# Optimization experiments

Hardware: AMD Instinct MI355X
Metric: run time of the kernel (lower is better)

Reference implementation:

```python
import jax, jax.numpy as jnp
import numpy as np

D_MODEL = 1024
NHEAD = 16
D_K = D_MODEL // NHEAD


def setup_inputs() -> dict:
    key = jax.random.key(0)
    ks = jax.random.split(key, 9)
    s = 1.0 / np.sqrt(D_MODEL)
    return {
        "x": jax.random.normal(ks[0], (4, 2048, D_MODEL), dtype=jnp.float32),
        "Wq": jax.random.uniform(ks[1], (D_MODEL, D_MODEL), jnp.float32, -s, s),
        "bq": jax.random.uniform(ks[2], (D_MODEL,), jnp.float32, -s, s),
        "Wk": jax.random.uniform(ks[3], (D_MODEL, D_MODEL), jnp.float32, -s, s),
        "bk": jax.random.uniform(ks[4], (D_MODEL,), jnp.float32, -s, s),
        "Wv": jax.random.uniform(ks[5], (D_MODEL, D_MODEL), jnp.float32, -s, s),
        "bv": jax.random.uniform(ks[6], (D_MODEL,), jnp.float32, -s, s),
        "Wo": jax.random.uniform(ks[7], (D_MODEL, D_MODEL), jnp.float32, -s, s),
        "bo": jax.random.uniform(ks[8], (D_MODEL,), jnp.float32, -s, s),
    }


def reference(x, Wq, bq, Wk, bk, Wv, bv, Wo, bo):
    B, S, D = x.shape
    H, dk = NHEAD, D_K

    def split_heads(t):  # [B,S,D] -> [B,H,S,dk]
        return t.reshape(B, S, H, dk).transpose(0, 2, 1, 3)

    q = split_heads(x @ Wq + bq)
    k = split_heads(x @ Wk + bk)
    v = split_heads(x @ Wv + bv)

    scores = jnp.einsum('bhqd,bhkd->bhqk', q, k) / jnp.sqrt(jnp.float32(dk))
    attn = jax.nn.softmax(scores, axis=-1)
    out = jnp.einsum('bhqk,bhkd->bhqd', attn, v)  # [B,H,S,dk]
    out = out.transpose(0, 2, 1, 3).reshape(B, S, D)
    return out @ Wo + bo
```

## Files before the change

### kernel.cpp

```cpp
#include <hip/hip_runtime.h>


typedef short short8 __attribute__((ext_vector_type(8)));
typedef float f32x4 __attribute__((ext_vector_type(4)));
typedef float f32x16 __attribute__((ext_vector_type(16)));

#define DMODEL 1024
#define NH 16
#define DK 64
#define SEQ 2048
#define NB 4
#define MTOT (NB*SEQ)
#define KSCALE 0.18033688f

__device__ __forceinline__ unsigned short f2bf(float f) {
    union { float f; unsigned u; } v; v.f = f;
    unsigned r = (v.u + 0x7FFFu + ((v.u >> 16) & 1u)) >> 16;
    return (unsigned short)r;
}

__device__ __forceinline__ unsigned pk2(float a, float b) {
    unsigned r;
    asm("v_cvt_pk_bf16_f32 %0, %1, %2" : "=v"(r) : "v"(a), "v"(b));
    return r;
}

__device__ __forceinline__ float exp2a(float x) {
    float r; asm("v_exp_f32 %0, %1" : "=v"(r) : "v"(x)); return r;
}

__device__ __forceinline__ float max3a(float a, float b, float c) {
    float r; asm("v_max3_f32 %0, %1, %2, %3" : "=v"(r) : "v"(a), "v"(b), "v"(c)); return r;
}

__device__ __forceinline__ void plswap(unsigned &a, unsigned &b) {
    asm volatile("v_permlane32_swap_b32 %0, %1" : "+v"(a), "+v"(b));
}

__device__ __forceinline__ void gload16(const short* g, short* l) {
    __builtin_amdgcn_global_load_lds(
        (const __attribute__((address_space(1))) unsigned*)(const void*)g,
        (__attribute__((address_space(3))) unsigned*)(void*)l,
        16, 0, 0);
}

union Frag { short8 s8; unsigned u[4]; };

__global__ __launch_bounds__(256) void cvt_kernel(const float* __restrict__ in,
                                                  short* __restrict__ out, int n4) {
    int i = blockIdx.x * 256 + threadIdx.x;
    if (i >= n4) return;
    float4 v = ((const float4*)in)[i];
    short4 o;
    o.x = (short)f2bf(v.x); o.y = (short)f2bf(v.y);
    o.z = (short)f2bf(v.z); o.w = (short)f2bf(v.w);
    ((short4*)out)[i] = o;
}

__global__ __launch_bounds__(256) void transpose_kernel(const float* __restrict__ W,
                                                        short* __restrict__ Wt) {
    __shared__ float t[32][33];
    int r0 = blockIdx.y * 32, c0 = blockIdx.x * 32;
    int tr = threadIdx.x >> 3;
    int tc = (threadIdx.x & 7) * 4;
    float4 v = *(const float4*)&W[(r0 + tr) * DMODEL + c0 + tc];
    t[tr][tc + 0] = v.x; t[tr][tc + 1] = v.y; t[tr][tc + 2] = v.z; t[tr][tc + 3] = v.w;
    __syncthreads();
    short4 o;
    o.x = (short)f2bf(t[tc + 0][tr]);
    o.y = (short)f2bf(t[tc + 1][tr]);
    o.z = (short)f2bf(t[tc + 2][tr]);
    o.w = (short)f2bf(t[tc + 3][tr]);
    *(short4*)&Wt[(c0 + tr) * DMODEL + r0 + tc] = o;
}

template<int MODE>
__global__ __launch_bounds__(256) void gemm_kernel(
    const short* __restrict__ A, const short* __restrict__ Bt,
    const float* __restrict__ b0, const float* __restrict__ b1, const float* __restrict__ b2,
    short* __restrict__ Qb, short* __restrict__ Kb, short* __restrict__ Vtb,
    float* __restrict__ Cout)
{
    __shared__ __align__(16) short As[128 * 64];
    __shared__ __align__(16) short Bs[128 * 64];
    const int K = DMODEL;
    int m0 = blockIdx.y * 128, n0 = blockIdx.x * 128;
    int tid = threadIdx.x, lane = tid & 63, wid = tid >> 6;
    int wm = (wid >> 1) * 64, wn = (wid & 1) * 64;

    int srow = 8 * wid + (lane >> 3);
    int scol = ((lane & 7) ^ (lane >> 3)) * 8;
    const short* aSrc = A + (size_t)(m0 + srow) * K + scol;
    const short* bSrc = Bt + (size_t)(n0 + srow) * K + scol;

    f32x4 acc[4][4];
    #pragma unroll
    for (int i = 0; i < 4; i++)
        #pragma unroll
        for (int j = 0; j < 4; j++) acc[i][j] = (f32x4){0.f, 0.f, 0.f, 0.f};

    for (int kt = 0; kt < K; kt += 64) {
        #pragma unroll
        for (int i = 0; i < 4; ++i) {
            gload16(aSrc + (size_t)(32 * i) * K + kt, &As[(8 * wid + 32 * i) * 64]);
            gload16(bSrc + (size_t)(32 * i) * K + kt, &Bs[(8 * wid + 32 * i) * 64]);
        }
        __syncthreads();
        #pragma unroll
        for (int kk = 0; kk < 2; ++kk) {
            int ko = kk * 32 + (lane >> 4) * 8;
            short8 af[4], bfv[4];
            #pragma unroll
            for (int i = 0; i < 4; i++) {
                int r = wm + i * 16 + (lane & 15);
                af[i] = *(const short8*)&As[(r * 64 + ko) ^ ((r & 7) << 3)];
            }
            #pragma unroll
            for (int j = 0; j < 4; j++) {
                int r = wn + j * 16 + (lane & 15);
                bfv[j] = *(const short8*)&Bs[(r * 64 + ko) ^ ((r & 7) << 3)];
            }
            #pragma unroll
            for (int i = 0; i < 4; i++)
                #pragma unroll
                for (int j = 0; j < 4; j++)
                    acc[i][j] = __builtin_amdgcn_mfma_f32_16x16x32_bf16(af[i], bfv[j], acc[i][j], 0, 0, 0);
        }
        __syncthreads();
    }

    #pragma unroll
    for (int i = 0; i < 4; i++) {
        #pragma unroll
        for (int j = 0; j < 4; j++) {
            int col = n0 + wn + j * 16 + (lane & 15);
            #pragma unroll
            for (int r = 0; r < 4; r++) {
                int row = m0 + wm + i * 16 + (lane >> 4) * 4 + r;
                float v = acc[i][j][r];
                if (MODE == 0) {
                    int seg = col >> 10, c = col & 1023;
                    const float* bp = (seg == 0) ? b0 : (seg == 1 ? b1 : b2);
                    v += bp[c];
                    if (seg == 1) v *= KSCALE;
                    unsigned short bv = f2bf(v);
                    int hh = c >> 6, d = c & 63, bb = row >> 11, s = row & 2047;
                    if (seg == 0)      Qb [(((bb * NH + hh) * SEQ) + s) * DK + d] = (short)bv;
                    else if (seg == 1) Kb [(((bb * NH + hh) * SEQ) + s) * DK + d] = (short)bv;
                    else               Vtb[(((bb * NH + hh) * DK) + d) * SEQ + s] = (short)bv;
                } else {
                    Cout[row * DMODEL + col] = v + b0[col];
                }
            }
        }
    }
}

__global__ __launch_bounds__(256) void attn_kernel(
    const short* __restrict__ Qb, const short* __restrict__ Kb,
    const short* __restrict__ Vtb, short* __restrict__ AOb)
{
    __shared__ __align__(16) short Ks[64 * 64];
    __shared__ __align__(16) short Vs[64 * 64];
    char* ksb = (char*)Ks;
    char* vsb = (char*)Vs;

    int bid = blockIdx.x;
    int wk = (bid & 7) * 128 + (bid >> 3);
    int qi = wk & 15, bh = wk >> 4;
    int h = bh & (NH - 1), b = bh >> 4;
    int q0 = qi * 128;

    int tid = threadIdx.x, lane = tid & 63, wid = tid >> 6;
    int hi = lane >> 5, l31 = lane & 31, l7 = lane & 7;
    const short* Qp = Qb + (size_t)bh * SEQ * DK;
    const short* Kp = Kb + (size_t)bh * SEQ * DK;
    const short* Vp = Vtb + (size_t)bh * DK * SEQ;

    short8 qf[4];
    #pragma unroll
    for (int ks = 0; ks < 4; ks++)
        qf[ks] = *(const short8*)&Qp[(q0 + wid * 32 + l31) * DK + ks * 16 + hi * 8];

    f32x16 ot0, ot1;
    #pragma unroll
    for (int r = 0; r < 16; r++) { ot0[r] = 0.f; ot1[r] = 0.f; }
    float mrun = -1e30f, lrun = 0.f;

    int srow = tid >> 3, ssl = tid & 7;
    #pragma unroll
    for (int i = 0; i < 2; i++) {
        int row = srow + 32 * i;
        *(short8*)(ksb + ((row * 128 + ssl * 16) ^ ((row & 7) << 4))) =
            *(const short8*)&Kp[row * DK + ssl * 8];
        *(short8*)(vsb + ((row * 128 + ssl * 16) ^ ((row & 7) << 4))) =
            *(const short8*)&Vp[row * SEQ + ssl * 8];
    }
    __syncthreads();

    const int NT = SEQ / 64;
    for (int t = 0; t < NT; ++t) {
        short8 nk[2], nv[2];
        if (t + 1 < NT) {
            int kv0n = (t + 1) * 64;
            #pragma unroll
            for (int i = 0; i < 2; i++) {
                int row = srow + 32 * i;
                nk[i] = *(const short8*)&Kp[(kv0n + row) * DK + ssl * 8];
                nv[i] = *(const short8*)&Vp[row * SEQ + kv0n + ssl * 8];
            }
        }

        f32x16 st0, st1;
        #pragma unroll
        for (int r = 0; r < 16; r++) { st0[r] = 0.f; st1[r] = 0.f; }
        __builtin_amdgcn_s_setprio(1);
        #pragma unroll
        for (int ks = 0; ks < 4; ks++) {
            short8 kf0 = *(const short8*)(ksb + ((l31 * 128 + ks * 32 + hi * 16) ^ (l7 << 4)));
            short8 kf1 = *(const short8*)(ksb + (((32 + l31) * 128 + ks * 32 + hi * 16) ^ (l7 << 4)));
            st0 = __builtin_amdgcn_mfma_f32_32x32x16_bf16(kf0, qf[ks], st0, 0, 0, 0);
            st1 = __builtin_amdgcn_mfma_f32_32x32x16_bf16(kf1, qf[ks], st1, 0, 0, 0);
        }
        __builtin_amdgcn_s_setprio(0);

        float m8[8];
        #pragma unroll
        for (int i = 0; i < 8; i++) m8[i] = max3a(st0[i], st0[i + 8], st1[i]);
        float m4[4];
        #pragma unroll
        for (int i = 0; i < 4; i++) m4[i] = max3a(m8[i], m8[i + 4], st1[i + 8]);
        float m2a = max3a(m4[0], m4[2], st1[12]);
        float m2b = max3a(m4[1], m4[3], st1[13]);
        float mxv = max3a(m2a, m2b, st1[14]);
        mxv = fmaxf(mxv, st1[15]);
        float mt = fmaxf(mxv, __shfl_xor(mxv, 32, 64));

        if (!__all(mt - mrun <= 11.0f)) {
            float mn = fmaxf(mrun, mt);
            float al = exp2a(mrun - mn);
            lrun *= al;
            #pragma unroll
            for (int r = 0; r < 16; r++) { ot0[r] *= al; ot1[r] *= al; }
            mrun = mn;
        }
        #pragma unroll
        for (int r = 0; r < 16; r++) {
            st0[r] = exp2a(st0[r] - mrun);
            st1[r] = exp2a(st1[r] - mrun);
        }
        float s16[16];
        #pragma unroll
        for (int r = 0; r < 16; r++) s16[r] = st0[r] + st1[r];
        #pragma unroll
        for (int s = 8; s > 0; s >>= 1)
            #pragma unroll
            for (int r = 0; r < 8; r++) if (r < s) s16[r] += s16[r + s];
        lrun += s16[0] + __shfl_xor(s16[0], 32, 64);

        unsigned w0[8], w1[8];
        #pragma unroll
        for (int m = 0; m < 4; m++) {
            w0[m * 2]     = pk2(st0[4 * m], st0[4 * m + 1]);
            w0[m * 2 + 1] = pk2(st0[4 * m + 2], st0[4 * m + 3]);
            w1[m * 2]     = pk2(st1[4 * m], st1[4 * m + 1]);
            w1[m * 2 + 1] = pk2(st1[4 * m + 2], st1[4 * m + 3]);
        }
        short8 pf[4];
        #pragma unroll
        for (int ks = 0; ks < 4; ks++) {
            unsigned a0 = (ks < 2) ? w0[4 * (ks & 1) + 0] : w1[4 * (ks & 1) + 0];
            unsigned b0_ = (ks < 2) ? w0[4 * (ks & 1) + 2] : w1[4 * (ks & 1) + 2];
            unsigned a1 = (ks < 2) ? w0[4 * (ks & 1) + 1] : w1[4 * (ks & 1) + 1];
            unsigned b1_ = (ks < 2) ? w0[4 * (ks & 1) + 3] : w1[4 * (ks & 1) + 3];
            plswap(a0, b0_);
            plswap(a1, b1_);
            Frag f;
            f.u[0] = a0; f.u[1] = a1; f.u[2] = b0_; f.u[3] = b1_;
            pf[ks] = f.s8;
        }

        __builtin_amdgcn_s_setprio(1);
        #pragma unroll
        for (int ks = 0; ks < 4; ks++) {
            short8 vf0 = *(const short8*)(vsb + ((l31 * 128 + ks * 32 + hi * 16) ^ (l7 << 4)));
            short8 vf1 = *(const short8*)(vsb + (((32 + l31) * 128 + ks * 32 + hi * 16) ^ (l7 << 4)));
            ot0 = __builtin_amdgcn_mfma_f32_32x32x16_bf16(vf0, pf[ks], ot0, 0, 0, 0);
            ot1 = __builtin_amdgcn_mfma_f32_32x32x16_bf16(vf1, pf[ks], ot1, 0, 0, 0);
        }
        __builtin_amdgcn_s_setprio(0);

        __syncthreads();
        if (t + 1 < NT) {
            #pragma unroll
            for (int i = 0; i < 2; i++) {
                int row = srow + 32 * i;
                *(short8*)(ksb + ((row * 128 + ssl * 16) ^ ((row & 7) << 4))) = nk[i];
                *(short8*)(vsb + ((row * 128 + ssl * 16) ^ ((row & 7) << 4))) = nv[i];
            }
        }
        __syncthreads();
    }

    float inv = 1.f / lrun;
    int srow_q = b * SEQ + q0 + wid * 32 + l31;
    short* outp = AOb + (size_t)srow_q * DMODEL + h * DK;
    #pragma unroll
    for (int g = 0; g < 4; g++) {
        int d0 = 8 * g + 4 * hi;
        uint2 u;
        u.x = pk2(ot0[4 * g] * inv, ot0[4 * g + 1] * inv);
        u.y = pk2(ot0[4 * g + 2] * inv, ot0[4 * g + 3] * inv);
        *(uint2*)&outp[d0] = u;
        uint2 v2;
        v2.x = pk2(ot1[4 * g] * inv, ot1[4 * g + 1] * inv);
        v2.y = pk2(ot1[4 * g + 2] * inv, ot1[4 * g + 3] * inv);
        *(uint2*)&outp[32 + d0] = v2;
    }
}

extern "C" void kernel_launch(void* const* d_in, const int* in_sizes, int n_in,
                              void* d_out, int out_size, void* d_ws, size_t ws_size,
                              hipStream_t stream)
{
    const float* x  = (const float*)d_in[0];
    const float* Wq = (const float*)d_in[1];
    const float* bq = (const float*)d_in[2];
    const float* Wk = (const float*)d_in[3];
    const float* bk = (const float*)d_in[4];
    const float* Wv = (const float*)d_in[5];
    const float* bv = (const float*)d_in[6];
    const float* Wo = (const float*)d_in[7];
    const float* bo = (const float*)d_in[8];
    float* out = (float*)d_out;

    char* w = (char*)d_ws;
    short* xb    = (short*)w; w += (size_t)MTOT * DMODEL * 2;
    short* Wqkvt = (short*)w; w += (size_t)3 * DMODEL * DMODEL * 2;
    short* Wot   = (short*)w; w += (size_t)DMODEL * DMODEL * 2;
    short* Qb    = (short*)w; w += (size_t)MTOT * DMODEL * 2;
    short* Kb    = (short*)w; w += (size_t)MTOT * DMODEL * 2;
    short* Vtb   = (short*)w; w += (size_t)MTOT * DMODEL * 2;
    short* AOb   = (short*)w; w += (size_t)MTOT * DMODEL * 2;

    cvt_kernel<<<(MTOT * DMODEL / 4 + 255) / 256, 256, 0, stream>>>(x, xb, MTOT * DMODEL / 4);

    dim3 tg(32, 32);
    transpose_kernel<<<tg, 256, 0, stream>>>(Wq, Wqkvt);
    transpose_kernel<<<tg, 256, 0, stream>>>(Wk, Wqkvt + DMODEL * DMODEL);
    transpose_kernel<<<tg, 256, 0, stream>>>(Wv, Wqkvt + 2 * DMODEL * DMODEL);
    transpose_kernel<<<tg, 256, 0, stream>>>(Wo, Wot);

    gemm_kernel<0><<<dim3(3 * DMODEL / 128, MTOT / 128), 256, 0, stream>>>(
        xb, Wqkvt, bq, bk, bv, Qb, Kb, Vtb, nullptr);

    attn_kernel<<<dim3(SEQ / 128 * NH * NB), 256, 0, stream>>>(Qb, Kb, Vtb, AOb);

    gemm_kernel<1><<<dim3(DMODEL / 128, MTOT / 128), 256, 0, stream>>>(
        AOb, Wot, bo, nullptr, nullptr, nullptr, nullptr, nullptr, out);
}
```

Measured before the change: 226.3 us.

## Fuse prep kernels, double-buffer attention K/V tiles, fold max offset into MFMA init

```diff
diff --git a/kernel.cpp b/kernel.cpp
--- a/kernel.cpp
+++ b/kernel.cpp
@@ -37,6 +37,19 @@
     asm volatile("v_permlane32_swap_b32 %0, %1" : "+v"(a), "+v"(b));
 }
 
+__device__ __forceinline__ float pairmax32(float v) {
+    float x = v, y;
+    asm volatile("v_mov_b32 %0, %1" : "=v"(y) : "v"(v));
+    asm volatile("v_permlane32_swap_b32 %0, %1" : "+v"(x), "+v"(y));
+    return fmaxf(x, y);
+}
+__device__ __forceinline__ float pairsum32(float v) {
+    float x = v, y;
+    asm volatile("v_mov_b32 %0, %1" : "=v"(y) : "v"(v));
+    asm volatile("v_permlane32_swap_b32 %0, %1" : "+v"(x), "+v"(y));
+    return x + y;
+}
+
 __device__ __forceinline__ void gload16(const short* g, short* l) {
     __builtin_amdgcn_global_load_lds(
         (const __attribute__((address_space(1))) unsigned*)(const void*)g,
@@ -46,21 +59,29 @@
 
 union Frag { short8 s8; unsigned u[4]; };
 
-__global__ __launch_bounds__(256) void cvt_kernel(const float* __restrict__ in,
-                                                  short* __restrict__ out, int n4) {
-    int i = blockIdx.x * 256 + threadIdx.x;
-    if (i >= n4) return;
-    float4 v = ((const float4*)in)[i];
-    short4 o;
-    o.x = (short)f2bf(v.x); o.y = (short)f2bf(v.y);
-    o.z = (short)f2bf(v.z); o.w = (short)f2bf(v.w);
-    ((short4*)out)[i] = o;
-}
-
-__global__ __launch_bounds__(256) void transpose_kernel(const float* __restrict__ W,
-                                                        short* __restrict__ Wt) {
+#define NCVT (MTOT * DMODEL / 4 / 256)
+__global__ __launch_bounds__(256) void prep_kernel(
+    const float* __restrict__ x, short* __restrict__ xb,
+    const float* __restrict__ Wq, const float* __restrict__ Wk,
+    const float* __restrict__ Wv, const float* __restrict__ Wo,
+    short* __restrict__ Wqkvt, short* __restrict__ Wot)
+{
     __shared__ float t[32][33];
-    int r0 = blockIdx.y * 32, c0 = blockIdx.x * 32;
+    int bid = blockIdx.x;
+    if (bid < NCVT) {
+        int i = bid * 256 + threadIdx.x;
+        float4 v = ((const float4*)x)[i];
+        short4 o;
+        o.x = (short)f2bf(v.x); o.y = (short)f2bf(v.y);
+        o.z = (short)f2bf(v.z); o.w = (short)f2bf(v.w);
+        ((short4*)xb)[i] = o;
+        return;
+    }
+    int wb = bid - NCVT;
+    int widx = wb >> 10, tile = wb & 1023;
+    const float* W = (widx == 0) ? Wq : (widx == 1) ? Wk : (widx == 2) ? Wv : Wo;
+    short* dst = (widx < 3) ? (Wqkvt + (size_t)widx * DMODEL * DMODEL) : Wot;
+    int r0 = (tile >> 5) * 32, c0 = (tile & 31) * 32;
     int tr = threadIdx.x >> 3;
     int tc = (threadIdx.x & 7) * 4;
     float4 v = *(const float4*)&W[(r0 + tr) * DMODEL + c0 + tc];
@@ -71,7 +92,7 @@
     o.y = (short)f2bf(t[tc + 1][tr]);
     o.z = (short)f2bf(t[tc + 2][tr]);
     o.w = (short)f2bf(t[tc + 3][tr]);
-    *(short4*)&Wt[(c0 + tr) * DMODEL + r0 + tc] = o;
+    *(short4*)&dst[(c0 + tr) * DMODEL + r0 + tc] = o;
 }
 
 template<int MODE>
@@ -160,10 +181,8 @@
     const short* __restrict__ Qb, const short* __restrict__ Kb,
     const short* __restrict__ Vtb, short* __restrict__ AOb)
 {
-    __shared__ __align__(16) short Ks[64 * 64];
-    __shared__ __align__(16) short Vs[64 * 64];
-    char* ksb = (char*)Ks;
-    char* vsb = (char*)Vs;
+    __shared__ __align__(16) short Ks[2][64 * 64];
+    __shared__ __align__(16) short Vs[2][64 * 64];
 
     int bid = blockIdx.x;
     int wk = (bid & 7) * 128 + (bid >> 3);
@@ -185,21 +204,25 @@
     f32x16 ot0, ot1;
     #pragma unroll
     for (int r = 0; r < 16; r++) { ot0[r] = 0.f; ot1[r] = 0.f; }
-    float mrun = -1e30f, lrun = 0.f;
+    float mrun = 0.f, lrun = 0.f;
 
     int srow = tid >> 3, ssl = tid & 7;
     #pragma unroll
     for (int i = 0; i < 2; i++) {
         int row = srow + 32 * i;
-        *(short8*)(ksb + ((row * 128 + ssl * 16) ^ ((row & 7) << 4))) =
+        *(short8*)((char*)Ks[0] + ((row * 128 + ssl * 16) ^ ((row & 7) << 4))) =
             *(const short8*)&Kp[row * DK + ssl * 8];
-        *(short8*)(vsb + ((row * 128 + ssl * 16) ^ ((row & 7) << 4))) =
+        *(short8*)((char*)Vs[0] + ((row * 128 + ssl * 16) ^ ((row & 7) << 4))) =
             *(const short8*)&Vp[row * SEQ + ssl * 8];
     }
     __syncthreads();
 
     const int NT = SEQ / 64;
     for (int t = 0; t < NT; ++t) {
+        int cur = t & 1;
+        const char* kb = (const char*)Ks[cur];
+        const char* vb = (const char*)Vs[cur];
+
         short8 nk[2], nv[2];
         if (t + 1 < NT) {
             int kv0n = (t + 1) * 64;
@@ -211,14 +234,15 @@
             }
         }
 
+        float negm = -mrun;
         f32x16 st0, st1;
         #pragma unroll
-        for (int r = 0; r < 16; r++) { st0[r] = 0.f; st1[r] = 0.f; }
+        for (int r = 0; r < 16; r++) { st0[r] = negm; st1[r] = negm; }
         __builtin_amdgcn_s_setprio(1);
         #pragma unroll
         for (int ks = 0; ks < 4; ks++) {
-            short8 kf0 = *(const short8*)(ksb + ((l31 * 128 + ks * 32 + hi * 16) ^ (l7 << 4)));
-            short8 kf1 = *(const short8*)(ksb + (((32 + l31) * 128 + ks * 32 + hi * 16) ^ (l7 << 4)));
+            short8 kf0 = *(const short8*)(kb + ((l31 * 128 + ks * 32 + hi * 16) ^ (l7 << 4)));
+            short8 kf1 = *(const short8*)(kb + (((32 + l31) * 128 + ks * 32 + hi * 16) ^ (l7 << 4)));
             st0 = __builtin_amdgcn_mfma_f32_32x32x16_bf16(kf0, qf[ks], st0, 0, 0, 0);
             st1 = __builtin_amdgcn_mfma_f32_32x32x16_bf16(kf1, qf[ks], st1, 0, 0, 0);
         }
@@ -234,20 +258,23 @@
         float m2b = max3a(m4[1], m4[3], st1[13]);
         float mxv = max3a(m2a, m2b, st1[14]);
         mxv = fmaxf(mxv, st1[15]);
-        float mt = fmaxf(mxv, __shfl_xor(mxv, 32, 64));
-
-        if (!__all(mt - mrun <= 11.0f)) {
-            float mn = fmaxf(mrun, mt);
-            float al = exp2a(mrun - mn);
+        float mt = pairmax32(mxv);
+
+        if (!__all(mt <= 11.0f)) {
+            float d = fmaxf(mt, 0.f);
+            float al = exp2a(-d);
             lrun *= al;
             #pragma unroll
-            for (int r = 0; r < 16; r++) { ot0[r] *= al; ot1[r] *= al; }
-            mrun = mn;
+            for (int r = 0; r < 16; r++) {
+                ot0[r] *= al; ot1[r] *= al;
+                st0[r] -= d; st1[r] -= d;
+            }
+            mrun += d;
         }
         #pragma unroll
         for (int r = 0; r < 16; r++) {
-            st0[r] = exp2a(st0[r] - mrun);
-            st1[r] = exp2a(st1[r] - mrun);
+            st0[r] = exp2a(st0[r]);
+            st1[r] = exp2a(st1[r]);
         }
         float s16[16];
         #pragma unroll
@@ -256,7 +283,7 @@
         for (int s = 8; s > 0; s >>= 1)
             #pragma unroll
             for (int r = 0; r < 8; r++) if (r < s) s16[r] += s16[r + s];
-        lrun += s16[0] + __shfl_xor(s16[0], 32, 64);
+        lrun += pairsum32(s16[0]);
 
         unsigned w0[8], w1[8];
         #pragma unroll
@@ -283,20 +310,21 @@
         __builtin_amdgcn_s_setprio(1);
         #pragma unroll
         for (int ks = 0; ks < 4; ks++) {
-            short8 vf0 = *(const short8*)(vsb + ((l31 * 128 + ks * 32 + hi * 16) ^ (l7 << 4)));
-            short8 vf1 = *(const short8*)(vsb + (((32 + l31) * 128 + ks * 32 + hi * 16) ^ (l7 << 4)));
+            short8 vf0 = *(const short8*)(vb + ((l31 * 128 + ks * 32 + hi * 16) ^ (l7 << 4)));
+            short8 vf1 = *(const short8*)(vb + (((32 + l31) * 128 + ks * 32 + hi * 16) ^ (l7 << 4)));
             ot0 = __builtin_amdgcn_mfma_f32_32x32x16_bf16(vf0, pf[ks], ot0, 0, 0, 0);
             ot1 = __builtin_amdgcn_mfma_f32_32x32x16_bf16(vf1, pf[ks], ot1, 0, 0, 0);
         }
         __builtin_amdgcn_s_setprio(0);
 
-        __syncthreads();
         if (t + 1 < NT) {
+            char* kw = (char*)Ks[cur ^ 1];
+            char* vw = (char*)Vs[cur ^ 1];
             #pragma unroll
             for (int i = 0; i < 2; i++) {
                 int row = srow + 32 * i;
-                *(short8*)(ksb + ((row * 128 + ssl * 16) ^ ((row & 7) << 4))) = nk[i];
-                *(short8*)(vsb + ((row * 128 + ssl * 16) ^ ((row & 7) << 4))) = nv[i];
+                *(short8*)(kw + ((row * 128 + ssl * 16) ^ ((row & 7) << 4))) = nk[i];
+                *(short8*)(vw + ((row * 128 + ssl * 16) ^ ((row & 7) << 4))) = nv[i];
             }
         }
         __syncthreads();
@@ -343,13 +371,7 @@
     short* Vtb   = (short*)w; w += (size_t)MTOT * DMODEL * 2;
     short* AOb   = (short*)w; w += (size_t)MTOT * DMODEL * 2;
 
-    cvt_kernel<<<(MTOT * DMODEL / 4 + 255) / 256, 256, 0, stream>>>(x, xb, MTOT * DMODEL / 4);
-
-    dim3 tg(32, 32);
-    transpose_kernel<<<tg, 256, 0, stream>>>(Wq, Wqkvt);
-    transpose_kernel<<<tg, 256, 0, stream>>>(Wk, Wqkvt + DMODEL * DMODEL);
-    transpose_kernel<<<tg, 256, 0, stream>>>(Wv, Wqkvt + 2 * DMODEL * DMODEL);
-    transpose_kernel<<<tg, 256, 0, stream>>>(Wo, Wot);
+    prep_kernel<<<NCVT + 4096, 256, 0, stream>>>(x, xb, Wq, Wk, Wv, Wo, Wqkvt, Wot);
 
     gemm_kernel<0><<<dim3(3 * DMODEL / 128, MTOT / 128), 256, 0, stream>>>(
         xb, Wqkvt, bq, bk, bv, Qb, Kb, Vtb, nullptr);
```

Measured after the change: 224.3 us. No clear change (-0.9%).
